# Performance work log

Hardware: AMD Instinct MI355X
Metric: run time of the kernel (lower is better)

## Reference

```python
import jax, jax.numpy as jnp
import numpy as np

NEG_SLOPE_MLP = 0.1   # F.leaky_relu(x, 0.1) used throughout the repo
NEG_SLOPE_GAT = 0.2   # PyG GATv2Conv default negative_slope
HEADS = 2
OUT = 8


def lrelu(x):
    return jax.nn.leaky_relu(x, NEG_SLOPE_MLP)


def gatv2_conv(x, src, dst, e_attr, wl, bl, wr, br, we, att, bias):
    """PyG-style GATv2Conv with edge features, concat heads.
    x: [N, Din], src/dst: [E], e_attr: [E, 2]
    wl/wr: [heads*out, Din], we: [heads*out, 2], att: [heads, out], bias: [heads*out]
    """
    N = x.shape[0]
    xl = (x @ wl.T + bl).reshape(N, HEADS, OUT)   # source transform
    xr = (x @ wr.T + br).reshape(N, HEADS, OUT)   # target transform
    e = (e_attr @ we.T).reshape(-1, HEADS, OUT)
    m = jax.nn.leaky_relu(xl[src] + xr[dst] + e, NEG_SLOPE_GAT)   # [E, H, O]
    logits = jnp.einsum('ehd,hd->eh', m, att)                      # [E, H]
    # numerically-stable segment softmax over incoming edges of each dst node
    mx = jax.ops.segment_max(logits, dst, num_segments=N)          # [N, H]
    a = jnp.exp(logits - mx[dst])
    denom = jax.ops.segment_sum(a, dst, num_segments=N)
    alpha = a / (denom[dst] + 1e-16)                               # [E, H]
    out = jax.ops.segment_sum(xl[src] * alpha[..., None], dst, num_segments=N)
    return out.reshape(N, HEADS * OUT) + bias                      # [N, 16]


def setup_inputs() -> dict:
    key = jax.random.key(0)
    ks = iter(jax.random.split(key, 64))
    N, E = 250000, 5000000
    inp = {
        'x': jax.random.normal(next(ks), (N, 3), jnp.float32),
        'edge_index': jax.random.randint(next(ks), (2, E), 0, N, jnp.int32),
        'edge_attr': jax.random.normal(next(ks), (E, 2), jnp.float32),
        'meta_data': jax.random.normal(next(ks), (6,), jnp.float32),
    }
    shapes = dict(
        ft1_w=(8, 3), ft1_b=(8,), ft2_w=(8, 8), ft2_b=(8,),
        g1_wl=(16, 8), g1_bl=(16,), g1_wr=(16, 8), g1_br=(16,), g1_we=(16, 2), g1_att=(2, 8), g1_bias=(16,),
        g2_wl=(16, 16), g2_bl=(16,), g2_wr=(16, 16), g2_br=(16,), g2_we=(16, 2), g2_att=(2, 8), g2_bias=(16,),
        sp1_w=(64, 16), sp1_b=(64,), sp2_w=(16, 64), sp2_b=(16,),
        me_w=(8, 6), me_b=(8,),
        fc1_w=(24, 24), fc1_b=(24,), fc2_w=(8, 24), fc2_b=(8,), fc3_w=(3, 8), fc3_b=(3,),
    )
    for name, shp in shapes.items():
        inp[name] = 0.2 * jax.random.normal(next(ks), shp, jnp.float32)
    return inp


def reference(x, edge_index, edge_attr, meta_data,
              ft1_w, ft1_b, ft2_w, ft2_b,
              g1_wl, g1_bl, g1_wr, g1_br, g1_we, g1_att, g1_bias,
              g2_wl, g2_bl, g2_wr, g2_br, g2_we, g2_att, g2_bias,
              sp1_w, sp1_b, sp2_w, sp2_b, me_w, me_b,
              fc1_w, fc1_b, fc2_w, fc2_b, fc3_w, fc3_b):
    src, dst = edge_index[0], edge_index[1]
    # tiny per-node MLP feature transform
    h = lrelu(x @ ft1_w.T + ft1_b)
    h = lrelu(h @ ft2_w.T + ft2_b)                              # [N, 8]
    # 2-layer GATv2 block (activation between layers)
    h = gatv2_conv(h, src, dst, edge_attr, g1_wl, g1_bl, g1_wr, g1_br, g1_we, g1_att, g1_bias)
    h = lrelu(h)
    h = gatv2_conv(h, src, dst, edge_attr, g2_wl, g2_bl, g2_wr, g2_br, g2_we, g2_att, g2_bias)  # [N, 16]
    # sum pool over all nodes + small MLP
    p = h.sum(axis=0)                                           # [16]
    p = lrelu(p @ sp1_w.T + sp1_b)
    p = p @ sp2_w.T + sp2_b                                     # [16]
    # meta data encoder
    m = lrelu(meta_data @ me_w.T + me_b)                        # [8]
    z = jnp.concatenate([p, m], axis=0)                         # [24]
    z = lrelu(z @ fc1_w.T + fc1_b)
    z = lrelu(z @ fc2_w.T + fc2_b)
    # dropout is identity in eval/reference mode
    z = z @ fc3_w.T + fc3_b                                     # [3]
    return jax.nn.softmax(z[None, :], axis=1)                   # [1, 3]
```

## Files before the change

### kernel.cpp

```cpp
#include <hip/hip_runtime.h>
#include <hip/hip_bf16.h>
#include <hip/hip_fp16.h>
#include <math.h>


#define HO 16
#define BSHIFT 8
#define BNODES 256
#define PT 512
#define PCHUNK 6144
#define CAP2 6016

typedef __attribute__((ext_vector_type(2))) float v2f;

__device__ __forceinline__ float lrelu(float x, float s) { return x > 0.f ? x : s * x; }

__device__ __forceinline__ uint2 pack_fp8x8(const float* v) {
    int a = __builtin_amdgcn_cvt_pk_fp8_f32(v[0], v[1], 0, false);
    a     = __builtin_amdgcn_cvt_pk_fp8_f32(v[2], v[3], a, true);
    int b = __builtin_amdgcn_cvt_pk_fp8_f32(v[4], v[5], 0, false);
    b     = __builtin_amdgcn_cvt_pk_fp8_f32(v[6], v[7], b, true);
    return make_uint2((unsigned int)a, (unsigned int)b);
}

__device__ __forceinline__ void unpack_fp8x8(uint2 u, float* v) {
    v2f f0 = __builtin_amdgcn_cvt_pk_f32_fp8((int)u.x, false);
    v2f f1 = __builtin_amdgcn_cvt_pk_f32_fp8((int)u.x, true);
    v2f f2 = __builtin_amdgcn_cvt_pk_f32_fp8((int)u.y, false);
    v2f f3 = __builtin_amdgcn_cvt_pk_f32_fp8((int)u.y, true);
    v[0]=f0.x; v[1]=f0.y; v[2]=f1.x; v[3]=f1.y;
    v[4]=f2.x; v[5]=f2.y; v[6]=f3.x; v[7]=f3.y;
}

__global__ void __launch_bounds__(256) node_l1(
    const float* __restrict__ x,
    const float* __restrict__ ft1_w, const float* __restrict__ ft1_b,
    const float* __restrict__ ft2_w, const float* __restrict__ ft2_b,
    const float* __restrict__ wl, const float* __restrict__ bl,
    const float* __restrict__ wr, const float* __restrict__ br,
    uint2* __restrict__ xlA, float* __restrict__ xr, int N)
{
    int n = blockIdx.x * 256 + threadIdx.x;
    if (n >= N) return;
    float x0 = x[3*n], x1 = x[3*n+1], x2 = x[3*n+2];
    float h1[8];
#pragma unroll
    for (int j = 0; j < 8; j++) {
        float a = ft1_w[3*j]*x0 + ft1_w[3*j+1]*x1 + ft1_w[3*j+2]*x2 + ft1_b[j];
        h1[j] = lrelu(a, 0.1f);
    }
    float h2[8];
#pragma unroll
    for (int j = 0; j < 8; j++) {
        float a = ft2_b[j];
#pragma unroll
        for (int k = 0; k < 8; k++) a += ft2_w[8*j+k]*h1[k];
        h2[j] = lrelu(a, 0.1f);
    }
    float ol[HO], orr[HO];
#pragma unroll
    for (int j = 0; j < HO; j++) {
        float a = bl[j], b = br[j];
#pragma unroll
        for (int k = 0; k < 8; k++) { a += wl[8*j+k]*h2[k]; b += wr[8*j+k]*h2[k]; }
        ol[j] = a; orr[j] = b;
    }
    uint2 p0 = pack_fp8x8(ol);
    uint2 p1 = pack_fp8x8(ol + 8);
    ((uint4*)xlA)[n] = make_uint4(p0.x, p0.y, p1.x, p1.y);
    float4* xr4 = (float4*)(xr + (size_t)n*HO);
#pragma unroll
    for (int q = 0; q < 4; q++)
        xr4[q] = make_float4(orr[4*q], orr[4*q+1], orr[4*q+2], orr[4*q+3]);
}

__global__ void __launch_bounds__(256) k_binit(int* __restrict__ bcur)
{
    int b = blockIdx.x * 256 + threadIdx.x;
    if (b < 1024) bcur[b] = b * CAP2;
}

__global__ void __launch_bounds__(PT) k_part(
    const int* __restrict__ src, const int* __restrict__ dst,
    const float* __restrict__ eattr, int* __restrict__ bcur,
    uint2* __restrict__ grecs, int E)
{
    __shared__ int hist[1024], lofs[1024], gofs[1024], lcur[1024];
    __shared__ int scan_s[PT];
    __shared__ uint2 srecs[PCHUNK];
    __shared__ unsigned short bid[PCHUNK];
    int t = threadIdx.x;
    int base = blockIdx.x * PCHUNK;
    int cnt = E - base; if (cnt > PCHUNK) cnt = PCHUNK;

    for (int b = t; b < 1024; b += PT) hist[b] = 0;
    __syncthreads();
    for (int i = t; i < cnt; i += PT)
        atomicAdd(&hist[dst[base + i] >> BSHIFT], 1);
    __syncthreads();
    int h0 = hist[2*t], h1 = hist[2*t+1];
    int pair = h0 + h1;
    scan_s[t] = pair;
    __syncthreads();
    for (int off = 1; off < PT; off <<= 1) {
        int add = (t >= off) ? scan_s[t - off] : 0;
        __syncthreads();
        scan_s[t] += add;
        __syncthreads();
    }
    int pbase = scan_s[t] - pair;
    lofs[2*t]   = pbase;
    lofs[2*t+1] = pbase + h0;
    __syncthreads();
    for (int b = t; b < 1024; b += PT) {
        int c = hist[b];
        int g = (c > 0) ? atomicAdd(&bcur[b], c) : 0;
        gofs[b] = g - lofs[b];
        lcur[b] = 0;
    }
    __syncthreads();
    for (int i = t; i < cnt; i += PT) {
        int e = base + i;
        int d = dst[e];
        int b = d >> BSHIFT;
        float2 ea = ((const float2*)eattr)[e];
        __half2 hv = __floats2half2_rn(ea.x, ea.y);
        unsigned int eb = *reinterpret_cast<unsigned int*>(&hv);
        int q = atomicAdd(&lcur[b], 1);
        int idx = lofs[b] + q;
        srecs[idx] = make_uint2(((unsigned int)src[e] << 8) | (unsigned int)(d & (BNODES-1)), eb);
        bid[idx] = (unsigned short)b;
    }
    __syncthreads();
    for (int i = t; i < cnt; i += PT) {
        int b = bid[i];
        int pos = gofs[b] + i;
        if (pos < (b + 1) * CAP2) grecs[pos] = srecs[i];
    }
}

__global__ void __launch_bounds__(256) k_fine(
    const int* __restrict__ bcur, uint2* recs,
    int* __restrict__ rowS, int* __restrict__ rowE, int N)
{
    __shared__ uint2 rout[CAP2];
    __shared__ int lhist[256], lsc[256], lcur2[256];
    int b = blockIdx.x;
    int bstart = b * CAP2;
    int cnt = bcur[b] - bstart;
    if (cnt > CAP2) cnt = CAP2;
    if (cnt < 0) cnt = 0;
    int t = threadIdx.x;
    lhist[t] = 0;
    __syncthreads();
    for (int i = t; i < cnt; i += 256)
        atomicAdd(&lhist[recs[bstart + i].x & (BNODES-1)], 1);
    __syncthreads();
    int v = lhist[t];
    lsc[t] = v;
    __syncthreads();
    for (int off = 1; off < 256; off <<= 1) {
        int add = (t >= off) ? lsc[t - off] : 0;
        __syncthreads();
        lsc[t] += add;
        __syncthreads();
    }
    int ex = lsc[t] - v;
    lcur2[t] = ex;
    int n = (b << BSHIFT) + t;
    if (n < N) { rowS[n] = bstart + ex; rowE[n] = bstart + ex + v; }
    __syncthreads();
    for (int i = t; i < cnt; i += 256) {
        uint2 r = recs[bstart + i];
        int p = atomicAdd(&lcur2[r.x & (BNODES-1)], 1);
        rout[p] = make_uint2(r.x >> 8, r.y);
    }
    __syncthreads();
    for (int i = t; i < cnt; i += 256)
        recs[bstart + i] = rout[i];
}

struct AggState { float m, s, acc[8]; };

__device__ __forceinline__ void agg_edge(
    AggState& st, const float* va, const float* xd,
    const float* w0, const float* w1, const float* at,
    float ea0, float ea1)
{
    float lg = 0.f;
#pragma unroll
    for (int o = 0; o < 8; o++) {
        float mv = va[o] + xd[o] + (w0[o]*ea0 + w1[o]*ea1);
        mv = mv > 0.f ? mv : 0.2f*mv;
        lg += mv * at[o];
    }
    float nm = fmaxf(st.m, lg);
    float sc = __expf(st.m - nm);
    float wv = __expf(lg - nm);
    st.s = st.s*sc + wv;
#pragma unroll
    for (int o = 0; o < 8; o++) st.acc[o] = st.acc[o]*sc + wv*va[o];
    st.m = nm;
}

__device__ __forceinline__ void agg_node_head(
    int n, int h,
    const int* __restrict__ rowS, const int* __restrict__ rowE,
    const uint2* __restrict__ recs,
    const uint2* __restrict__ xl8, const float* __restrict__ xr,
    const float* __restrict__ we, const float* __restrict__ att,
    const float* __restrict__ bias, float* out)
{
    int kb = h*8;
    float xd[8], w0[8], w1[8], at[8];
    {
        const float4* xrp = (const float4*)(xr + (size_t)n*HO + kb);
        float4 d0 = xrp[0], d1 = xrp[1];
        xd[0]=d0.x; xd[1]=d0.y; xd[2]=d0.z; xd[3]=d0.w;
        xd[4]=d1.x; xd[5]=d1.y; xd[6]=d1.z; xd[7]=d1.w;
    }
#pragma unroll
    for (int o = 0; o < 8; o++) {
        w0[o] = we[2*(kb+o)];
        w1[o] = we[2*(kb+o)+1];
        at[o] = att[kb+o];
    }
    AggState st;
    st.m = -INFINITY; st.s = 0.f;
#pragma unroll
    for (int o = 0; o < 8; o++) st.acc[o] = 0.f;

    int i = rowS[n], end = rowE[n];
    for (; i + 4 <= end; i += 4) {
        uint2 rA = recs[i], rB = recs[i+1], rC = recs[i+2], rD = recs[i+3];
        uint2 gA = xl8[(size_t)rA.x*2 + h];
        uint2 gB = xl8[(size_t)rB.x*2 + h];
        uint2 gC = xl8[(size_t)rC.x*2 + h];
        uint2 gD = xl8[(size_t)rD.x*2 + h];
        float vA[8], vB[8], vC[8], vD[8];
        unpack_fp8x8(gA, vA); unpack_fp8x8(gB, vB);
        unpack_fp8x8(gC, vC); unpack_fp8x8(gD, vD);
        __half2 hA = *reinterpret_cast<__half2*>(&rA.y);
        __half2 hB = *reinterpret_cast<__half2*>(&rB.y);
        __half2 hC = *reinterpret_cast<__half2*>(&rC.y);
        __half2 hD = *reinterpret_cast<__half2*>(&rD.y);
        agg_edge(st, vA, xd, w0, w1, at, __low2float(hA), __high2float(hA));
        agg_edge(st, vB, xd, w0, w1, at, __low2float(hB), __high2float(hB));
        agg_edge(st, vC, xd, w0, w1, at, __low2float(hC), __high2float(hC));
        agg_edge(st, vD, xd, w0, w1, at, __low2float(hD), __high2float(hD));
    }
    for (; i < end; i++) {
        uint2 rA = recs[i];
        uint2 gA = xl8[(size_t)rA.x*2 + h];
        float vA[8];
        unpack_fp8x8(gA, vA);
        __half2 hA = *reinterpret_cast<__half2*>(&rA.y);
        agg_edge(st, vA, xd, w0, w1, at, __low2float(hA), __high2float(hA));
    }
    float inv = 1.f/(st.s + 1e-16f);
#pragma unroll
    for (int o = 0; o < 8; o++) out[o] = st.acc[o]*inv + bias[kb+o];
}

__global__ void __launch_bounds__(256) node_agg_l1(
    const int* __restrict__ rowS, const int* __restrict__ rowE,
    const uint2* __restrict__ recs,
    const uint2* __restrict__ xlA, float* xr,
    const float* __restrict__ we, const float* __restrict__ att,
    const float* __restrict__ bias,
    const float* __restrict__ wl2, const float* __restrict__ bl2,
    const float* __restrict__ wr2, const float* __restrict__ br2,
    uint2* __restrict__ xlB, int N)
{
    int tid = blockIdx.x * 256 + threadIdx.x;
    int n = tid >> 1, h = tid & 1;
    if (n >= N) return;
    int kb = h*8;
    float out[8];
    agg_node_head(n, h, rowS, rowE, recs, xlA, xr, we, att, bias, out);
    float hh[8];
#pragma unroll
    for (int o = 0; o < 8; o++) hh[o] = lrelu(out[o], 0.1f);
    float hfull[HO];
#pragma unroll
    for (int o = 0; o < 8; o++) {
        float hp = __shfl_xor(hh[o], 1, 64);
        hfull[kb + o] = hh[o];
        hfull[(kb ^ 8) + o] = hp;
    }
    float ol[8], orr[8];
#pragma unroll
    for (int jo = 0; jo < 8; jo++) {
        int j = kb + jo;
        float a = bl2[j], b = br2[j];
#pragma unroll
        for (int k = 0; k < HO; k++) { a += wl2[HO*j+k]*hfull[k]; b += wr2[HO*j+k]*hfull[k]; }
        ol[jo] = a; orr[jo] = b;
    }
    xlB[(size_t)n*2 + h] = pack_fp8x8(ol);
    float4* xr4 = (float4*)(xr + (size_t)n*HO + kb);
    xr4[0] = make_float4(orr[0], orr[1], orr[2], orr[3]);
    xr4[1] = make_float4(orr[4], orr[5], orr[6], orr[7]);
}

__global__ void __launch_bounds__(256) node_agg_l2(
    const int* __restrict__ rowS, const int* __restrict__ rowE,
    const uint2* __restrict__ recs,
    const uint2* __restrict__ xlB, const float* __restrict__ xr,
    const float* __restrict__ we, const float* __restrict__ att,
    const float* __restrict__ bias, float* __restrict__ partials, int pstride, int N)
{
    int tid = blockIdx.x * 256 + threadIdx.x;
    int n = tid >> 1, h = tid & 1;
    float out[8];
    if (n < N) {
        agg_node_head(n, h, rowS, rowE, recs, xlB, xr, we, att, bias, out);
    } else {
#pragma unroll
        for (int o = 0; o < 8; o++) out[o] = 0.f;
    }
#pragma unroll
    for (int off = 32; off >= 2; off >>= 1) {
#pragma unroll
        for (int o = 0; o < 8; o++) out[o] += __shfl_down(out[o], off, 64);
    }
    __shared__ float sm[4][2][8];
    int wave = threadIdx.x >> 6, lane = threadIdx.x & 63;
    if (lane < 2) {
#pragma unroll
        for (int o = 0; o < 8; o++) sm[wave][lane][o] = out[o];
    }
    __syncthreads();
    if (threadIdx.x < 16) {
        int hh = threadIdx.x >> 3, oo = threadIdx.x & 7;
        float t = sm[0][hh][oo] + sm[1][hh][oo] + sm[2][hh][oo] + sm[3][hh][oo];
        partials[(size_t)(hh*8 + oo) * pstride + blockIdx.x] = t;
    }
}

__global__ void __launch_bounds__(256) k_reduce(
    const float* __restrict__ partials, int pstride, int nparts,
    float* __restrict__ pool)
{
    __shared__ float s[256];
    int c = blockIdx.x;
    int t = threadIdx.x;
    const float* col = partials + (size_t)c * pstride;
    float acc = 0.f;
    for (int r = t; r < nparts; r += 256) acc += col[r];
    s[t] = acc;
    __syncthreads();
#pragma unroll
    for (int off = 128; off > 0; off >>= 1) {
        if (t < off) s[t] += s[t + off];
        __syncthreads();
    }
    if (t == 0) pool[c] = s[0];
}

__global__ void __launch_bounds__(64) final_mlp(
    const float* __restrict__ pool, const float* __restrict__ meta,
    const float* __restrict__ sp1_w, const float* __restrict__ sp1_b,
    const float* __restrict__ sp2_w, const float* __restrict__ sp2_b,
    const float* __restrict__ me_w, const float* __restrict__ me_b,
    const float* __restrict__ fc1_w, const float* __restrict__ fc1_b,
    const float* __restrict__ fc2_w, const float* __restrict__ fc2_b,
    const float* __restrict__ fc3_w, const float* __restrict__ fc3_b,
    float* __restrict__ out)
{
    __shared__ float s1[64], zb[24], z1[24], z2[8];
    int t = threadIdx.x;
    {
        float acc = sp1_b[t];
        for (int k = 0; k < 16; k++) acc += pool[k]*sp1_w[t*16+k];
        s1[t] = lrelu(acc, 0.1f);
    }
    __syncthreads();
    if (t < 16) {
        float acc = sp2_b[t];
        for (int k = 0; k < 64; k++) acc += s1[k]*sp2_w[t*64+k];
        zb[t] = acc;
    } else if (t < 24) {
        int j = t - 16;
        float acc = me_b[j];
        for (int k = 0; k < 6; k++) acc += meta[k]*me_w[j*6+k];
        zb[t] = lrelu(acc, 0.1f);
    }
    __syncthreads();
    if (t < 24) {
        float acc = fc1_b[t];
        for (int k = 0; k < 24; k++) acc += zb[k]*fc1_w[t*24+k];
        z1[t] = lrelu(acc, 0.1f);
    }
    __syncthreads();
    if (t < 8) {
        float acc = fc2_b[t];
        for (int k = 0; k < 24; k++) acc += z1[k]*fc2_w[t*24+k];
        z2[t] = lrelu(acc, 0.1f);
    }
    __syncthreads();
    if (t == 0) {
        float z3[3]; float mxv = -1e30f;
        for (int j = 0; j < 3; j++) {
            float acc = fc3_b[j];
            for (int k = 0; k < 8; k++) acc += z2[k]*fc3_w[j*8+k];
            z3[j] = acc; mxv = fmaxf(mxv, acc);
        }
        float s = 0.f;
        for (int j = 0; j < 3; j++) { z3[j] = __expf(z3[j]-mxv); s += z3[j]; }
        for (int j = 0; j < 3; j++) out[j] = z3[j]/s;
    }
}

extern "C" void kernel_launch(void* const* d_in, const int* in_sizes, int n_in,
                              void* d_out, int out_size, void* d_ws, size_t ws_size,
                              hipStream_t stream)
{
    const float* x      = (const float*)d_in[0];
    const int*   eidx   = (const int*)  d_in[1];
    const float* eattr  = (const float*)d_in[2];
    const float* meta   = (const float*)d_in[3];
    const float* ft1_w  = (const float*)d_in[4];
    const float* ft1_b  = (const float*)d_in[5];
    const float* ft2_w  = (const float*)d_in[6];
    const float* ft2_b  = (const float*)d_in[7];
    const float* g1_wl  = (const float*)d_in[8];
    const float* g1_bl  = (const float*)d_in[9];
    const float* g1_wr  = (const float*)d_in[10];
    const float* g1_br  = (const float*)d_in[11];
    const float* g1_we  = (const float*)d_in[12];
    const float* g1_att = (const float*)d_in[13];
    const float* g1_bias= (const float*)d_in[14];
    const float* g2_wl  = (const float*)d_in[15];
    const float* g2_bl  = (const float*)d_in[16];
    const float* g2_wr  = (const float*)d_in[17];
    const float* g2_br  = (const float*)d_in[18];
    const float* g2_we  = (const float*)d_in[19];
    const float* g2_att = (const float*)d_in[20];
    const float* g2_bias= (const float*)d_in[21];
    const float* sp1_w  = (const float*)d_in[22];
    const float* sp1_b  = (const float*)d_in[23];
    const float* sp2_w  = (const float*)d_in[24];
    const float* sp2_b  = (const float*)d_in[25];
    const float* me_w   = (const float*)d_in[26];
    const float* me_b   = (const float*)d_in[27];
    const float* fc1_w  = (const float*)d_in[28];
    const float* fc1_b  = (const float*)d_in[29];
    const float* fc2_w  = (const float*)d_in[30];
    const float* fc2_b  = (const float*)d_in[31];
    const float* fc3_w  = (const float*)d_in[32];
    const float* fc3_b  = (const float*)d_in[33];
    float* out = (float*)d_out;

    const int N = in_sizes[0] / 3;
    const int E = in_sizes[2] / 2;
    const int* src = eidx;
    const int* dst = eidx + E;

    const int BN    = (N + 255) / 256;
    const int BN2   = (2*N + 255) / 256;
    const int NBUCK = (N + BNODES - 1) >> BSHIFT;
    const int BP    = (E + PCHUNK - 1) / PCHUNK;
    const int pstride = (BN2 + 63) & ~63;

    char* w = (char*)d_ws;
    size_t off = 0;
    auto take = [&](size_t bytes) { size_t o = off; off += (bytes + 255) & ~(size_t)255; return o; };
    int*    rowS     = (int*)   (w + take((size_t)4*N));
    int*    rowE     = (int*)   (w + take((size_t)4*N));
    int*    bcur     = (int*)   (w + take(4096));
    float*  pool     = (float*) (w + take(64));
    float*  partials = (float*) (w + take((size_t)4*16*pstride));
    uint2*  recs     = (uint2*) (w + take((size_t)8*NBUCK*CAP2));
    uint2*  xlA      = (uint2*) (w + take((size_t)16*N));
    uint2*  xlB      = (uint2*) (w + take((size_t)16*N));
    float*  xr       = (float*) (w + take((size_t)64*N));

    node_l1<<<BN, 256, 0, stream>>>(x, ft1_w, ft1_b, ft2_w, ft2_b,
                                    g1_wl, g1_bl, g1_wr, g1_br, xlA, xr, N);
    k_binit<<<4, 256, 0, stream>>>(bcur);
    k_part<<<BP, PT, 0, stream>>>(src, dst, eattr, bcur, recs, E);
    k_fine<<<NBUCK, 256, 0, stream>>>(bcur, recs, rowS, rowE, N);

    node_agg_l1<<<BN2, 256, 0, stream>>>(rowS, rowE, recs, xlA, xr,
                                         g1_we, g1_att, g1_bias,
                                         g2_wl, g2_bl, g2_wr, g2_br, xlB, N);
    node_agg_l2<<<BN2, 256, 0, stream>>>(rowS, rowE, recs, xlB, xr,
                                         g2_we, g2_att, g2_bias, partials, pstride, N);
    k_reduce<<<16, 256, 0, stream>>>(partials, pstride, BN2, pool);
    final_mlp<<<1, 64, 0, stream>>>(pool, meta, sp1_w, sp1_b, sp2_w, sp2_b,
                                    me_w, me_b, fc1_w, fc1_b, fc2_w, fc2_b,
                                    fc3_w, fc3_b, out);
}
```

Measured before the change: 424.7 us.

## Split each node-head edge loop across four lanes with online-softmax merge

The aggregation kernels now give each (node, head) pair four lanes instead of one. Each lane processes a strided subset of the incoming edges and keeps a partial online-softmax state, and the partial states are combined with xor-shuffle merges. The second-layer projection is split so that each sub-lane computes two output channels, and the fp8 pieces are assembled through shuffles. Non-temporal loads and stores are added for the edge records and xr. The aim is more parallelism and memory-level concurrency on the degree-20 gather loops, at the cost of extra shuffle/exp merge work and a larger grid and partials array.

```diff
diff --git a/kernel.cpp b/kernel.cpp
--- a/kernel.cpp
+++ b/kernel.cpp
@@ -12,6 +12,8 @@
 #define CAP2 6016
 
 typedef __attribute__((ext_vector_type(2))) float v2f;
+typedef __attribute__((ext_vector_type(4))) float v4f;
+typedef __attribute__((ext_vector_type(2))) unsigned int v2u;
 
 __device__ __forceinline__ float lrelu(float x, float s) { return x > 0.f ? x : s * x; }
 
@@ -32,6 +34,11 @@
     v[4]=f2.x; v[5]=f2.y; v[6]=f3.x; v[7]=f3.y;
 }
 
+__device__ __forceinline__ uint2 ntload_u2(const uint2* p) {
+    v2u v = __builtin_nontemporal_load((const v2u*)p);
+    return make_uint2(v.x, v.y);
+}
+
 __global__ void __launch_bounds__(256) node_l1(
     const float* __restrict__ x,
     const float* __restrict__ ft1_w, const float* __restrict__ ft1_b,
@@ -68,10 +75,12 @@
     uint2 p0 = pack_fp8x8(ol);
     uint2 p1 = pack_fp8x8(ol + 8);
     ((uint4*)xlA)[n] = make_uint4(p0.x, p0.y, p1.x, p1.y);
-    float4* xr4 = (float4*)(xr + (size_t)n*HO);
-#pragma unroll
-    for (int q = 0; q < 4; q++)
-        xr4[q] = make_float4(orr[4*q], orr[4*q+1], orr[4*q+2], orr[4*q+3]);
+    v4f* xr4 = (v4f*)(xr + (size_t)n*HO);
+#pragma unroll
+    for (int q = 0; q < 4; q++) {
+        v4f v; v.x = orr[4*q]; v.y = orr[4*q+1]; v.z = orr[4*q+2]; v.w = orr[4*q+3];
+        __builtin_nontemporal_store(v, xr4 + q);
+    }
 }
 
 __global__ void __launch_bounds__(256) k_binit(int* __restrict__ bcur)
@@ -203,19 +212,36 @@
     st.m = nm;
 }
 
-__device__ __forceinline__ void agg_node_head(
-    int n, int h,
+__device__ __forceinline__ void merge_xor(AggState& st, int mask)
+{
+    float pm = __shfl_xor(st.m, mask, 64);
+    float ps = __shfl_xor(st.s, mask, 64);
+    float pacc[8];
+#pragma unroll
+    for (int o = 0; o < 8; o++) pacc[o] = __shfl_xor(st.acc[o], mask, 64);
+    float nm = fmaxf(st.m, pm);
+    float e1 = __expf(st.m - nm);
+    float e2 = __expf(pm - nm);
+    st.s = st.s*e1 + ps*e2;
+#pragma unroll
+    for (int o = 0; o < 8; o++) st.acc[o] = st.acc[o]*e1 + pacc[o]*e2;
+    st.m = nm;
+}
+
+__device__ __forceinline__ void agg_partial(
+    int n, int h, int sub,
     const int* __restrict__ rowS, const int* __restrict__ rowE,
     const uint2* __restrict__ recs,
     const uint2* __restrict__ xl8, const float* __restrict__ xr,
     const float* __restrict__ we, const float* __restrict__ att,
-    const float* __restrict__ bias, float* out)
+    AggState& st)
 {
     int kb = h*8;
     float xd[8], w0[8], w1[8], at[8];
     {
-        const float4* xrp = (const float4*)(xr + (size_t)n*HO + kb);
-        float4 d0 = xrp[0], d1 = xrp[1];
+        const v4f* xrp = (const v4f*)(xr + (size_t)n*HO + kb);
+        v4f d0 = __builtin_nontemporal_load(xrp);
+        v4f d1 = __builtin_nontemporal_load(xrp + 1);
         xd[0]=d0.x; xd[1]=d0.y; xd[2]=d0.z; xd[3]=d0.w;
         xd[4]=d1.x; xd[5]=d1.y; xd[6]=d1.z; xd[7]=d1.w;
     }
@@ -225,41 +251,31 @@
         w1[o] = we[2*(kb+o)+1];
         at[o] = att[kb+o];
     }
-    AggState st;
-    st.m = -INFINITY; st.s = 0.f;
+    st.m = -1e30f; st.s = 0.f;
 #pragma unroll
     for (int o = 0; o < 8; o++) st.acc[o] = 0.f;
 
-    int i = rowS[n], end = rowE[n];
-    for (; i + 4 <= end; i += 4) {
-        uint2 rA = recs[i], rB = recs[i+1], rC = recs[i+2], rD = recs[i+3];
+    int i = rowS[n] + sub, end = rowE[n];
+    for (; i + 4 < end; i += 8) {
+        uint2 rA = ntload_u2(&recs[i]);
+        uint2 rB = ntload_u2(&recs[i+4]);
         uint2 gA = xl8[(size_t)rA.x*2 + h];
         uint2 gB = xl8[(size_t)rB.x*2 + h];
-        uint2 gC = xl8[(size_t)rC.x*2 + h];
-        uint2 gD = xl8[(size_t)rD.x*2 + h];
-        float vA[8], vB[8], vC[8], vD[8];
+        float vA[8], vB[8];
         unpack_fp8x8(gA, vA); unpack_fp8x8(gB, vB);
-        unpack_fp8x8(gC, vC); unpack_fp8x8(gD, vD);
         __half2 hA = *reinterpret_cast<__half2*>(&rA.y);
         __half2 hB = *reinterpret_cast<__half2*>(&rB.y);
-        __half2 hC = *reinterpret_cast<__half2*>(&rC.y);
-        __half2 hD = *reinterpret_cast<__half2*>(&rD.y);
         agg_edge(st, vA, xd, w0, w1, at, __low2float(hA), __high2float(hA));
         agg_edge(st, vB, xd, w0, w1, at, __low2float(hB), __high2float(hB));
-        agg_edge(st, vC, xd, w0, w1, at, __low2float(hC), __high2float(hC));
-        agg_edge(st, vD, xd, w0, w1, at, __low2float(hD), __high2float(hD));
-    }
-    for (; i < end; i++) {
-        uint2 rA = recs[i];
+    }
+    if (i < end) {
+        uint2 rA = ntload_u2(&recs[i]);
         uint2 gA = xl8[(size_t)rA.x*2 + h];
         float vA[8];
         unpack_fp8x8(gA, vA);
         __half2 hA = *reinterpret_cast<__half2*>(&rA.y);
         agg_edge(st, vA, xd, w0, w1, at, __low2float(hA), __high2float(hA));
     }
-    float inv = 1.f/(st.s + 1e-16f);
-#pragma unroll
-    for (int o = 0; o < 8; o++) out[o] = st.acc[o]*inv + bias[kb+o];
 }
 
 __global__ void __launch_bounds__(256) node_agg_l1(
@@ -273,34 +289,47 @@
     uint2* __restrict__ xlB, int N)
 {
     int tid = blockIdx.x * 256 + threadIdx.x;
-    int n = tid >> 1, h = tid & 1;
+    int n = tid >> 3, h = (tid >> 2) & 1, sub = tid & 3;
     if (n >= N) return;
     int kb = h*8;
-    float out[8];
-    agg_node_head(n, h, rowS, rowE, recs, xlA, xr, we, att, bias, out);
+    AggState st;
+    agg_partial(n, h, sub, rowS, rowE, recs, xlA, xr, we, att, st);
+    merge_xor(st, 1);
+    merge_xor(st, 2);
+    float inv = 1.f/(st.s + 1e-16f);
     float hh[8];
 #pragma unroll
-    for (int o = 0; o < 8; o++) hh[o] = lrelu(out[o], 0.1f);
+    for (int o = 0; o < 8; o++) hh[o] = lrelu(st.acc[o]*inv + bias[kb+o], 0.1f);
     float hfull[HO];
 #pragma unroll
     for (int o = 0; o < 8; o++) {
-        float hp = __shfl_xor(hh[o], 1, 64);
+        float hp = __shfl_xor(hh[o], 4, 64);
         hfull[kb + o] = hh[o];
         hfull[(kb ^ 8) + o] = hp;
     }
-    float ol[8], orr[8];
-#pragma unroll
-    for (int jo = 0; jo < 8; jo++) {
-        int j = kb + jo;
-        float a = bl2[j], b = br2[j];
-#pragma unroll
-        for (int k = 0; k < HO; k++) { a += wl2[HO*j+k]*hfull[k]; b += wr2[HO*j+k]*hfull[k]; }
-        ol[jo] = a; orr[jo] = b;
-    }
-    xlB[(size_t)n*2 + h] = pack_fp8x8(ol);
-    float4* xr4 = (float4*)(xr + (size_t)n*HO + kb);
-    xr4[0] = make_float4(orr[0], orr[1], orr[2], orr[3]);
-    xr4[1] = make_float4(orr[4], orr[5], orr[6], orr[7]);
+    int j0 = kb + 2*sub;
+    float a0 = bl2[j0], a1 = bl2[j0+1], b0 = br2[j0], b1 = br2[j0+1];
+#pragma unroll
+    for (int k = 0; k < HO; k++) {
+        float hk = hfull[k];
+        a0 += wl2[HO*j0 + k]     * hk;
+        a1 += wl2[HO*(j0+1) + k] * hk;
+        b0 += wr2[HO*j0 + k]     * hk;
+        b1 += wr2[HO*(j0+1) + k] * hk;
+    }
+    {
+        v2f v; v.x = b0; v.y = b1;
+        __builtin_nontemporal_store(v, (v2f*)(xr + (size_t)n*HO + kb + 2*sub));
+    }
+    int piece = __builtin_amdgcn_cvt_pk_fp8_f32(a0, a1, 0, false);
+    unsigned int pw = ((unsigned int)piece & 0xFFFFu) << ((sub & 1) * 16);
+    unsigned int px = (sub < 2) ? pw : 0u;
+    unsigned int py = (sub < 2) ? 0u : pw;
+    px |= (unsigned int)__shfl_xor((int)px, 1, 64);
+    py |= (unsigned int)__shfl_xor((int)py, 1, 64);
+    px |= (unsigned int)__shfl_xor((int)px, 2, 64);
+    py |= (unsigned int)__shfl_xor((int)py, 2, 64);
+    if (sub == 0) xlB[(size_t)n*2 + h] = make_uint2(px, py);
 }
 
 __global__ void __launch_bounds__(256) node_agg_l2(
@@ -311,24 +340,32 @@
     const float* __restrict__ bias, float* __restrict__ partials, int pstride, int N)
 {
     int tid = blockIdx.x * 256 + threadIdx.x;
-    int n = tid >> 1, h = tid & 1;
+    int n = tid >> 3, h = (tid >> 2) & 1, sub = tid & 3;
     float out[8];
+#pragma unroll
+    for (int o = 0; o < 8; o++) out[o] = 0.f;
     if (n < N) {
-        agg_node_head(n, h, rowS, rowE, recs, xlB, xr, we, att, bias, out);
-    } else {
-#pragma unroll
-        for (int o = 0; o < 8; o++) out[o] = 0.f;
-    }
-#pragma unroll
-    for (int off = 32; off >= 2; off >>= 1) {
+        AggState st;
+        agg_partial(n, h, sub, rowS, rowE, recs, xlB, xr, we, att, st);
+        merge_xor(st, 1);
+        merge_xor(st, 2);
+        if (sub == 0) {
+            float inv = 1.f/(st.s + 1e-16f);
+            int kb = h*8;
+#pragma unroll
+            for (int o = 0; o < 8; o++) out[o] = st.acc[o]*inv + bias[kb+o];
+        }
+    }
+#pragma unroll
+    for (int off = 32; off >= 8; off >>= 1) {
 #pragma unroll
         for (int o = 0; o < 8; o++) out[o] += __shfl_down(out[o], off, 64);
     }
     __shared__ float sm[4][2][8];
     int wave = threadIdx.x >> 6, lane = threadIdx.x & 63;
-    if (lane < 2) {
-#pragma unroll
-        for (int o = 0; o < 8; o++) sm[wave][lane][o] = out[o];
+    if (lane == 0 || lane == 4) {
+#pragma unroll
+        for (int o = 0; o < 8; o++) sm[wave][lane >> 2][o] = out[o];
     }
     __syncthreads();
     if (threadIdx.x < 16) {
@@ -458,10 +495,10 @@
     const int* dst = eidx + E;
 
     const int BN    = (N + 255) / 256;
-    const int BN2   = (2*N + 255) / 256;
+    const int BN8   = (8*N + 255) / 256;
     const int NBUCK = (N + BNODES - 1) >> BSHIFT;
     const int BP    = (E + PCHUNK - 1) / PCHUNK;
-    const int pstride = (BN2 + 63) & ~63;
+    const int pstride = (BN8 + 63) & ~63;
 
     char* w = (char*)d_ws;
     size_t off = 0;
@@ -482,12 +519,12 @@
     k_part<<<BP, PT, 0, stream>>>(src, dst, eattr, bcur, recs, E);
     k_fine<<<NBUCK, 256, 0, stream>>>(bcur, recs, rowS, rowE, N);
 
-    node_agg_l1<<<BN2, 256, 0, stream>>>(rowS, rowE, recs, xlA, xr,
+    node_agg_l1<<<BN8, 256, 0, stream>>>(rowS, rowE, recs, xlA, xr,
                                          g1_we, g1_att, g1_bias,
                                          g2_wl, g2_bl, g2_wr, g2_br, xlB, N);
-    node_agg_l2<<<BN2, 256, 0, stream>>>(rowS, rowE, recs, xlB, xr,
+    node_agg_l2<<<BN8, 256, 0, stream>>>(rowS, rowE, recs, xlB, xr,
                                          g2_we, g2_att, g2_bias, partials, pstride, N);
-    k_reduce<<<16, 256, 0, stream>>>(partials, pstride, BN2, pool);
+    k_reduce<<<16, 256, 0, stream>>>(partials, pstride, BN8, pool);
     final_mlp<<<1, 64, 0, stream>>>(pool, meta, sp1_w, sp1_b, sp2_w, sp2_b,
                                     me_w, me_b, fc1_w, fc1_b, fc2_w, fc2_b,
                                     fc3_w, fc3_b, out);
```

Measured after the change: 466.1 us. +9.7%, slower.

## Process both attention heads per thread and use nontemporal loads/stores

Applied to the files above, without the earlier changes.

The aggregation kernels now assign one thread per node instead of one per (node, head). Each edge record is read once and one 16-byte fp8 gather fetches both heads. This removes the duplicated record reads and the cross-lane shuffle between head threads, but halves the thread count and raises register pressure, which can reduce occupancy and latency hiding for the irregular gathers. Nontemporal hints are also added on the streamed edge records and the xr row loads/stores.

```diff
diff --git a/kernel.cpp b/kernel.cpp
--- a/kernel.cpp
+++ b/kernel.cpp
@@ -12,6 +12,8 @@
 #define CAP2 6016
 
 typedef __attribute__((ext_vector_type(2))) float v2f;
+typedef __attribute__((ext_vector_type(4))) float v4f;
+typedef __attribute__((ext_vector_type(2))) unsigned int v2u;
 
 __device__ __forceinline__ float lrelu(float x, float s) { return x > 0.f ? x : s * x; }
 
@@ -23,13 +25,24 @@
     return make_uint2((unsigned int)a, (unsigned int)b);
 }
 
-__device__ __forceinline__ void unpack_fp8x8(uint2 u, float* v) {
+__device__ __forceinline__ void unpack_fp8x16(uint4 u, float* v) {
     v2f f0 = __builtin_amdgcn_cvt_pk_f32_fp8((int)u.x, false);
     v2f f1 = __builtin_amdgcn_cvt_pk_f32_fp8((int)u.x, true);
     v2f f2 = __builtin_amdgcn_cvt_pk_f32_fp8((int)u.y, false);
     v2f f3 = __builtin_amdgcn_cvt_pk_f32_fp8((int)u.y, true);
-    v[0]=f0.x; v[1]=f0.y; v[2]=f1.x; v[3]=f1.y;
-    v[4]=f2.x; v[5]=f2.y; v[6]=f3.x; v[7]=f3.y;
+    v2f f4 = __builtin_amdgcn_cvt_pk_f32_fp8((int)u.z, false);
+    v2f f5 = __builtin_amdgcn_cvt_pk_f32_fp8((int)u.z, true);
+    v2f f6 = __builtin_amdgcn_cvt_pk_f32_fp8((int)u.w, false);
+    v2f f7 = __builtin_amdgcn_cvt_pk_f32_fp8((int)u.w, true);
+    v[0]=f0.x;  v[1]=f0.y;  v[2]=f1.x;  v[3]=f1.y;
+    v[4]=f2.x;  v[5]=f2.y;  v[6]=f3.x;  v[7]=f3.y;
+    v[8]=f4.x;  v[9]=f4.y;  v[10]=f5.x; v[11]=f5.y;
+    v[12]=f6.x; v[13]=f6.y; v[14]=f7.x; v[15]=f7.y;
+}
+
+__device__ __forceinline__ uint2 ntload_u2(const uint2* p) {
+    v2u v = __builtin_nontemporal_load((const v2u*)p);
+    return make_uint2(v.x, v.y);
 }
 
 __global__ void __launch_bounds__(256) node_l1(
@@ -68,10 +81,12 @@
     uint2 p0 = pack_fp8x8(ol);
     uint2 p1 = pack_fp8x8(ol + 8);
     ((uint4*)xlA)[n] = make_uint4(p0.x, p0.y, p1.x, p1.y);
-    float4* xr4 = (float4*)(xr + (size_t)n*HO);
-#pragma unroll
-    for (int q = 0; q < 4; q++)
-        xr4[q] = make_float4(orr[4*q], orr[4*q+1], orr[4*q+2], orr[4*q+3]);
+    v4f* xr4 = (v4f*)(xr + (size_t)n*HO);
+#pragma unroll
+    for (int q = 0; q < 4; q++) {
+        v4f v; v.x = orr[4*q]; v.y = orr[4*q+1]; v.z = orr[4*q+2]; v.w = orr[4*q+3];
+        __builtin_nontemporal_store(v, xr4 + q);
+    }
 }
 
 __global__ void __launch_bounds__(256) k_binit(int* __restrict__ bcur)
@@ -203,138 +218,163 @@
     st.m = nm;
 }
 
-__device__ __forceinline__ void agg_node_head(
-    int n, int h,
+__device__ __forceinline__ void agg_node_both(
+    int n,
     const int* __restrict__ rowS, const int* __restrict__ rowE,
     const uint2* __restrict__ recs,
-    const uint2* __restrict__ xl8, const float* __restrict__ xr,
+    const uint4* __restrict__ xl16, const float* __restrict__ xr,
     const float* __restrict__ we, const float* __restrict__ att,
-    const float* __restrict__ bias, float* out)
-{
-    int kb = h*8;
-    float xd[8], w0[8], w1[8], at[8];
+    AggState& s0, AggState& s1)
+{
+    float xd[16], w0[16], w1[16], at[16];
     {
-        const float4* xrp = (const float4*)(xr + (size_t)n*HO + kb);
-        float4 d0 = xrp[0], d1 = xrp[1];
-        xd[0]=d0.x; xd[1]=d0.y; xd[2]=d0.z; xd[3]=d0.w;
-        xd[4]=d1.x; xd[5]=d1.y; xd[6]=d1.z; xd[7]=d1.w;
-    }
-#pragma unroll
-    for (int o = 0; o < 8; o++) {
-        w0[o] = we[2*(kb+o)];
-        w1[o] = we[2*(kb+o)+1];
-        at[o] = att[kb+o];
-    }
-    AggState st;
-    st.m = -INFINITY; st.s = 0.f;
-#pragma unroll
-    for (int o = 0; o < 8; o++) st.acc[o] = 0.f;
+        const v4f* xrp = (const v4f*)(xr + (size_t)n*HO);
+#pragma unroll
+        for (int q = 0; q < 4; q++) {
+            v4f d = __builtin_nontemporal_load(xrp + q);
+            xd[4*q]=d.x; xd[4*q+1]=d.y; xd[4*q+2]=d.z; xd[4*q+3]=d.w;
+        }
+    }
+#pragma unroll
+    for (int o = 0; o < 16; o++) {
+        w0[o] = we[2*o];
+        w1[o] = we[2*o+1];
+        at[o] = att[o];
+    }
+    s0.m = -1e30f; s0.s = 0.f;
+    s1.m = -1e30f; s1.s = 0.f;
+#pragma unroll
+    for (int o = 0; o < 8; o++) { s0.acc[o] = 0.f; s1.acc[o] = 0.f; }
 
     int i = rowS[n], end = rowE[n];
     for (; i + 4 <= end; i += 4) {
-        uint2 rA = recs[i], rB = recs[i+1], rC = recs[i+2], rD = recs[i+3];
-        uint2 gA = xl8[(size_t)rA.x*2 + h];
-        uint2 gB = xl8[(size_t)rB.x*2 + h];
-        uint2 gC = xl8[(size_t)rC.x*2 + h];
-        uint2 gD = xl8[(size_t)rD.x*2 + h];
-        float vA[8], vB[8], vC[8], vD[8];
-        unpack_fp8x8(gA, vA); unpack_fp8x8(gB, vB);
-        unpack_fp8x8(gC, vC); unpack_fp8x8(gD, vD);
+        uint2 rA = ntload_u2(&recs[i]);
+        uint2 rB = ntload_u2(&recs[i+1]);
+        uint2 rC = ntload_u2(&recs[i+2]);
+        uint2 rD = ntload_u2(&recs[i+3]);
+        uint4 gA = xl16[rA.x];
+        uint4 gB = xl16[rB.x];
+        uint4 gC = xl16[rC.x];
+        uint4 gD = xl16[rD.x];
+        {
+            float v[16]; unpack_fp8x16(gA, v);
+            __half2 hA = *reinterpret_cast<__half2*>(&rA.y);
+            float e0 = __low2float(hA), e1 = __high2float(hA);
+            agg_edge(s0, v,     xd,     w0,     w1,     at,     e0, e1);
+            agg_edge(s1, v + 8, xd + 8, w0 + 8, w1 + 8, at + 8, e0, e1);
+        }
+        {
+            float v[16]; unpack_fp8x16(gB, v);
+            __half2 hB = *reinterpret_cast<__half2*>(&rB.y);
+            float e0 = __low2float(hB), e1 = __high2float(hB);
+            agg_edge(s0, v,     xd,     w0,     w1,     at,     e0, e1);
+            agg_edge(s1, v + 8, xd + 8, w0 + 8, w1 + 8, at + 8, e0, e1);
+        }
+        {
+            float v[16]; unpack_fp8x16(gC, v);
+            __half2 hC = *reinterpret_cast<__half2*>(&rC.y);
+            float e0 = __low2float(hC), e1 = __high2float(hC);
+            agg_edge(s0, v,     xd,     w0,     w1,     at,     e0, e1);
+            agg_edge(s1, v + 8, xd + 8, w0 + 8, w1 + 8, at + 8, e0, e1);
+        }
+        {
+            float v[16]; unpack_fp8x16(gD, v);
+            __half2 hD = *reinterpret_cast<__half2*>(&rD.y);
+            float e0 = __low2float(hD), e1 = __high2float(hD);
+            agg_edge(s0, v,     xd,     w0,     w1,     at,     e0, e1);
+            agg_edge(s1, v + 8, xd + 8, w0 + 8, w1 + 8, at + 8, e0, e1);
+        }
+    }
+    for (; i < end; i++) {
+        uint2 rA = ntload_u2(&recs[i]);
+        uint4 gA = xl16[rA.x];
+        float v[16]; unpack_fp8x16(gA, v);
         __half2 hA = *reinterpret_cast<__half2*>(&rA.y);
-        __half2 hB = *reinterpret_cast<__half2*>(&rB.y);
-        __half2 hC = *reinterpret_cast<__half2*>(&rC.y);
-        __half2 hD = *reinterpret_cast<__half2*>(&rD.y);
-        agg_edge(st, vA, xd, w0, w1, at, __low2float(hA), __high2float(hA));
-        agg_edge(st, vB, xd, w0, w1, at, __low2float(hB), __high2float(hB));
-        agg_edge(st, vC, xd, w0, w1, at, __low2float(hC), __high2float(hC));
-        agg_edge(st, vD, xd, w0, w1, at, __low2float(hD), __high2float(hD));
-    }
-    for (; i < end; i++) {
-        uint2 rA = recs[i];
-        uint2 gA = xl8[(size_t)rA.x*2 + h];
-        float vA[8];
-        unpack_fp8x8(gA, vA);
-        __half2 hA = *reinterpret_cast<__half2*>(&rA.y);
-        agg_edge(st, vA, xd, w0, w1, at, __low2float(hA), __high2float(hA));
-    }
-    float inv = 1.f/(st.s + 1e-16f);
-#pragma unroll
-    for (int o = 0; o < 8; o++) out[o] = st.acc[o]*inv + bias[kb+o];
+        float e0 = __low2float(hA), e1 = __high2float(hA);
+        agg_edge(s0, v,     xd,     w0,     w1,     at,     e0, e1);
+        agg_edge(s1, v + 8, xd + 8, w0 + 8, w1 + 8, at + 8, e0, e1);
+    }
 }
 
 __global__ void __launch_bounds__(256) node_agg_l1(
     const int* __restrict__ rowS, const int* __restrict__ rowE,
     const uint2* __restrict__ recs,
-    const uint2* __restrict__ xlA, float* xr,
+    const uint4* __restrict__ xlA, float* xr,
     const float* __restrict__ we, const float* __restrict__ att,
     const float* __restrict__ bias,
     const float* __restrict__ wl2, const float* __restrict__ bl2,
     const float* __restrict__ wr2, const float* __restrict__ br2,
-    uint2* __restrict__ xlB, int N)
-{
-    int tid = blockIdx.x * 256 + threadIdx.x;
-    int n = tid >> 1, h = tid & 1;
+    uint4* __restrict__ xlB, int N)
+{
+    int n = blockIdx.x * 256 + threadIdx.x;
     if (n >= N) return;
-    int kb = h*8;
-    float out[8];
-    agg_node_head(n, h, rowS, rowE, recs, xlA, xr, we, att, bias, out);
-    float hh[8];
-#pragma unroll
-    for (int o = 0; o < 8; o++) hh[o] = lrelu(out[o], 0.1f);
+    AggState s0, s1;
+    agg_node_both(n, rowS, rowE, recs, xlA, xr, we, att, s0, s1);
+    float inv0 = 1.f/(s0.s + 1e-16f);
+    float inv1 = 1.f/(s1.s + 1e-16f);
     float hfull[HO];
 #pragma unroll
     for (int o = 0; o < 8; o++) {
-        float hp = __shfl_xor(hh[o], 1, 64);
-        hfull[kb + o] = hh[o];
-        hfull[(kb ^ 8) + o] = hp;
-    }
-    float ol[8], orr[8];
-#pragma unroll
-    for (int jo = 0; jo < 8; jo++) {
-        int j = kb + jo;
+        hfull[o]     = lrelu(s0.acc[o]*inv0 + bias[o],     0.1f);
+        hfull[8 + o] = lrelu(s1.acc[o]*inv1 + bias[8 + o], 0.1f);
+    }
+    float ol[HO], orr[HO];
+#pragma unroll
+    for (int j = 0; j < HO; j++) {
         float a = bl2[j], b = br2[j];
 #pragma unroll
         for (int k = 0; k < HO; k++) { a += wl2[HO*j+k]*hfull[k]; b += wr2[HO*j+k]*hfull[k]; }
-        ol[jo] = a; orr[jo] = b;
-    }
-    xlB[(size_t)n*2 + h] = pack_fp8x8(ol);
-    float4* xr4 = (float4*)(xr + (size_t)n*HO + kb);
-    xr4[0] = make_float4(orr[0], orr[1], orr[2], orr[3]);
-    xr4[1] = make_float4(orr[4], orr[5], orr[6], orr[7]);
+        ol[j] = a; orr[j] = b;
+    }
+    uint2 q0 = pack_fp8x8(ol);
+    uint2 q1 = pack_fp8x8(ol + 8);
+    xlB[n] = make_uint4(q0.x, q0.y, q1.x, q1.y);
+    v4f* xr4 = (v4f*)(xr + (size_t)n*HO);
+#pragma unroll
+    for (int q = 0; q < 4; q++) {
+        v4f v; v.x = orr[4*q]; v.y = orr[4*q+1]; v.z = orr[4*q+2]; v.w = orr[4*q+3];
+        __builtin_nontemporal_store(v, xr4 + q);
+    }
 }
 
 __global__ void __launch_bounds__(256) node_agg_l2(
     const int* __restrict__ rowS, const int* __restrict__ rowE,
     const uint2* __restrict__ recs,
-    const uint2* __restrict__ xlB, const float* __restrict__ xr,
+    const uint4* __restrict__ xlB, const float* __restrict__ xr,
     const float* __restrict__ we, const float* __restrict__ att,
     const float* __restrict__ bias, float* __restrict__ partials, int pstride, int N)
 {
-    int tid = blockIdx.x * 256 + threadIdx.x;
-    int n = tid >> 1, h = tid & 1;
-    float out[8];
+    int n = blockIdx.x * 256 + threadIdx.x;
+    float out[HO];
+#pragma unroll
+    for (int o = 0; o < HO; o++) out[o] = 0.f;
     if (n < N) {
-        agg_node_head(n, h, rowS, rowE, recs, xlB, xr, we, att, bias, out);
-    } else {
-#pragma unroll
-        for (int o = 0; o < 8; o++) out[o] = 0.f;
-    }
-#pragma unroll
-    for (int off = 32; off >= 2; off >>= 1) {
-#pragma unroll
-        for (int o = 0; o < 8; o++) out[o] += __shfl_down(out[o], off, 64);
-    }
-    __shared__ float sm[4][2][8];
+        AggState s0, s1;
+        agg_node_both(n, rowS, rowE, recs, xlB, xr, we, att, s0, s1);
+        float inv0 = 1.f/(s0.s + 1e-16f);
+        float inv1 = 1.f/(s1.s + 1e-16f);
+#pragma unroll
+        for (int o = 0; o < 8; o++) {
+            out[o]     = s0.acc[o]*inv0 + bias[o];
+            out[8 + o] = s1.acc[o]*inv1 + bias[8 + o];
+        }
+    }
+#pragma unroll
+    for (int off = 32; off >= 1; off >>= 1) {
+#pragma unroll
+        for (int o = 0; o < HO; o++) out[o] += __shfl_down(out[o], off, 64);
+    }
+    __shared__ float sm[4][HO];
     int wave = threadIdx.x >> 6, lane = threadIdx.x & 63;
-    if (lane < 2) {
-#pragma unroll
-        for (int o = 0; o < 8; o++) sm[wave][lane][o] = out[o];
-    }
-    __syncthreads();
-    if (threadIdx.x < 16) {
-        int hh = threadIdx.x >> 3, oo = threadIdx.x & 7;
-        float t = sm[0][hh][oo] + sm[1][hh][oo] + sm[2][hh][oo] + sm[3][hh][oo];
-        partials[(size_t)(hh*8 + oo) * pstride + blockIdx.x] = t;
+    if (lane == 0) {
+#pragma unroll
+        for (int o = 0; o < HO; o++) sm[wave][o] = out[o];
+    }
+    __syncthreads();
+    if (threadIdx.x < HO) {
+        int oo = threadIdx.x;
+        float t = sm[0][oo] + sm[1][oo] + sm[2][oo] + sm[3][oo];
+        partials[(size_t)oo * pstride + blockIdx.x] = t;
     }
 }
 
@@ -458,10 +498,9 @@
     const int* dst = eidx + E;
 
     const int BN    = (N + 255) / 256;
-    const int BN2   = (2*N + 255) / 256;
     const int NBUCK = (N + BNODES - 1) >> BSHIFT;
     const int BP    = (E + PCHUNK - 1) / PCHUNK;
-    const int pstride = (BN2 + 63) & ~63;
+    const int pstride = (BN + 63) & ~63;
 
     char* w = (char*)d_ws;
     size_t off = 0;
@@ -472,22 +511,22 @@
     float*  pool     = (float*) (w + take(64));
     float*  partials = (float*) (w + take((size_t)4*16*pstride));
     uint2*  recs     = (uint2*) (w + take((size_t)8*NBUCK*CAP2));
-    uint2*  xlA      = (uint2*) (w + take((size_t)16*N));
-    uint2*  xlB      = (uint2*) (w + take((size_t)16*N));
+    uint4*  xlA      = (uint4*) (w + take((size_t)16*N));
+    uint4*  xlB      = (uint4*) (w + take((size_t)16*N));
     float*  xr       = (float*) (w + take((size_t)64*N));
 
     node_l1<<<BN, 256, 0, stream>>>(x, ft1_w, ft1_b, ft2_w, ft2_b,
-                                    g1_wl, g1_bl, g1_wr, g1_br, xlA, xr, N);
+                                    g1_wl, g1_bl, g1_wr, g1_br, (uint2*)xlA, xr, N);
     k_binit<<<4, 256, 0, stream>>>(bcur);
     k_part<<<BP, PT, 0, stream>>>(src, dst, eattr, bcur, recs, E);
     k_fine<<<NBUCK, 256, 0, stream>>>(bcur, recs, rowS, rowE, N);
 
-    node_agg_l1<<<BN2, 256, 0, stream>>>(rowS, rowE, recs, xlA, xr,
-                                         g1_we, g1_att, g1_bias,
-                                         g2_wl, g2_bl, g2_wr, g2_br, xlB, N);
-    node_agg_l2<<<BN2, 256, 0, stream>>>(rowS, rowE, recs, xlB, xr,
-                                         g2_we, g2_att, g2_bias, partials, pstride, N);
-    k_reduce<<<16, 256, 0, stream>>>(partials, pstride, BN2, pool);
+    node_agg_l1<<<BN, 256, 0, stream>>>(rowS, rowE, recs, xlA, xr,
+                                        g1_we, g1_att, g1_bias,
+                                        g2_wl, g2_bl, g2_wr, g2_br, xlB, N);
+    node_agg_l2<<<BN, 256, 0, stream>>>(rowS, rowE, recs, xlB, xr,
+                                        g2_we, g2_att, g2_bias, partials, pstride, N);
+    k_reduce<<<16, 256, 0, stream>>>(partials, pstride, BN, pool);
     final_mlp<<<1, 64, 0, stream>>>(pool, meta, sp1_w, sp1_b, sp2_w, sp2_b,
                                     me_w, me_b, fc1_w, fc1_b, fc2_w, fc2_b,
                                     fc3_w, fc3_b, out);
```

After: 441.0 us. +3.8%, slower.

## Stage block's edge gathers cooperatively into LDS before per-node softmax aggregation

Applied to the files above, without the earlier changes.

Each 128-node block now walks its contiguous CSR edge range in chunks. All 256 threads cooperatively load the edge records and gather the full 16-byte fp8 source feature rows into shared memory, so the gathers are coalesced and spread evenly. Each thread then reads its own node's edges for its head from LDS. This removes the per-thread serial dependent gather chains and the load imbalance from skewed degrees. The cost is extra syncthreads, LDS capacity limiting occupancy, and each gather now fetching both heads per edge.

```diff
diff --git a/kernel.cpp b/kernel.cpp
--- a/kernel.cpp
+++ b/kernel.cpp
@@ -10,8 +10,10 @@
 #define PT 512
 #define PCHUNK 6144
 #define CAP2 6016
+#define CAPB 1984
 
 typedef __attribute__((ext_vector_type(2))) float v2f;
+typedef __attribute__((ext_vector_type(4))) float v4f;
 
 __device__ __forceinline__ float lrelu(float x, float s) { return x > 0.f ? x : s * x; }
 
@@ -203,84 +205,90 @@
     st.m = nm;
 }
 
-__device__ __forceinline__ void agg_node_head(
-    int n, int h,
+__device__ __forceinline__ void agg_lds(
+    int t, int nblk0, int N,
     const int* __restrict__ rowS, const int* __restrict__ rowE,
-    const uint2* __restrict__ recs,
-    const uint2* __restrict__ xl8, const float* __restrict__ xr,
-    const float* __restrict__ we, const float* __restrict__ att,
-    const float* __restrict__ bias, float* out)
-{
-    int kb = h*8;
-    float xd[8], w0[8], w1[8], at[8];
-    {
-        const float4* xrp = (const float4*)(xr + (size_t)n*HO + kb);
-        float4 d0 = xrp[0], d1 = xrp[1];
-        xd[0]=d0.x; xd[1]=d0.y; xd[2]=d0.z; xd[3]=d0.w;
-        xd[4]=d1.x; xd[5]=d1.y; xd[6]=d1.z; xd[7]=d1.w;
-    }
-#pragma unroll
-    for (int o = 0; o < 8; o++) {
-        w0[o] = we[2*(kb+o)];
-        w1[o] = we[2*(kb+o)+1];
-        at[o] = att[kb+o];
-    }
-    AggState st;
-    st.m = -INFINITY; st.s = 0.f;
-#pragma unroll
-    for (int o = 0; o < 8; o++) st.acc[o] = 0.f;
-
-    int i = rowS[n], end = rowE[n];
-    for (; i + 4 <= end; i += 4) {
-        uint2 rA = recs[i], rB = recs[i+1], rC = recs[i+2], rD = recs[i+3];
-        uint2 gA = xl8[(size_t)rA.x*2 + h];
-        uint2 gB = xl8[(size_t)rB.x*2 + h];
-        uint2 gC = xl8[(size_t)rC.x*2 + h];
-        uint2 gD = xl8[(size_t)rD.x*2 + h];
-        float vA[8], vB[8], vC[8], vD[8];
-        unpack_fp8x8(gA, vA); unpack_fp8x8(gB, vB);
-        unpack_fp8x8(gC, vC); unpack_fp8x8(gD, vD);
-        __half2 hA = *reinterpret_cast<__half2*>(&rA.y);
-        __half2 hB = *reinterpret_cast<__half2*>(&rB.y);
-        __half2 hC = *reinterpret_cast<__half2*>(&rC.y);
-        __half2 hD = *reinterpret_cast<__half2*>(&rD.y);
-        agg_edge(st, vA, xd, w0, w1, at, __low2float(hA), __high2float(hA));
-        agg_edge(st, vB, xd, w0, w1, at, __low2float(hB), __high2float(hB));
-        agg_edge(st, vC, xd, w0, w1, at, __low2float(hC), __high2float(hC));
-        agg_edge(st, vD, xd, w0, w1, at, __low2float(hD), __high2float(hD));
-    }
-    for (; i < end; i++) {
-        uint2 rA = recs[i];
-        uint2 gA = xl8[(size_t)rA.x*2 + h];
-        float vA[8];
-        unpack_fp8x8(gA, vA);
-        __half2 hA = *reinterpret_cast<__half2*>(&rA.y);
-        agg_edge(st, vA, xd, w0, w1, at, __low2float(hA), __high2float(hA));
-    }
-    float inv = 1.f/(st.s + 1e-16f);
-#pragma unroll
-    for (int o = 0; o < 8; o++) out[o] = st.acc[o]*inv + bias[kb+o];
+    const uint2* __restrict__ recs, const uint4* __restrict__ xl16,
+    uint4* va_s, unsigned int* ea_s,
+    bool alive, int rs, int re, int h,
+    const float* xd, const float* w0, const float* w1, const float* at,
+    AggState& st)
+{
+    int nlast = nblk0 + 127; if (nlast > N - 1) nlast = N - 1;
+    int ebeg = rowS[nblk0];
+    int eend = rowE[nlast];
+    for (int cbase = ebeg; cbase < eend; cbase += CAPB) {
+        int ccnt = eend - cbase; if (ccnt > CAPB) ccnt = CAPB;
+        __syncthreads();
+        for (int j = t; j < ccnt; j += 256) {
+            uint2 r = recs[cbase + j];
+            va_s[j] = xl16[r.x];
+            ea_s[j] = r.y;
+        }
+        __syncthreads();
+        if (alive) {
+            int ls = rs > cbase ? rs : cbase;
+            int ce = cbase + ccnt;
+            int le = re < ce ? re : ce;
+            for (int i = ls; i < le; i++) {
+                int j = i - cbase;
+                const uint2* vp = reinterpret_cast<const uint2*>(va_s + j);
+                uint2 g = vp[h];
+                float v[8]; unpack_fp8x8(g, v);
+                unsigned int eb = ea_s[j];
+                __half2 h2 = *reinterpret_cast<__half2*>(&eb);
+                agg_edge(st, v, xd, w0, w1, at, __low2float(h2), __high2float(h2));
+            }
+        }
+    }
 }
 
 __global__ void __launch_bounds__(256) node_agg_l1(
     const int* __restrict__ rowS, const int* __restrict__ rowE,
     const uint2* __restrict__ recs,
-    const uint2* __restrict__ xlA, float* xr,
+    const uint4* __restrict__ xlA, float* xr,
     const float* __restrict__ we, const float* __restrict__ att,
     const float* __restrict__ bias,
     const float* __restrict__ wl2, const float* __restrict__ bl2,
     const float* __restrict__ wr2, const float* __restrict__ br2,
     uint2* __restrict__ xlB, int N)
 {
-    int tid = blockIdx.x * 256 + threadIdx.x;
+    __shared__ uint4 va_s[CAPB];
+    __shared__ unsigned int ea_s[CAPB];
+    int t = threadIdx.x;
+    int tid = blockIdx.x * 256 + t;
     int n = tid >> 1, h = tid & 1;
-    if (n >= N) return;
+    bool alive = (n < N);
     int kb = h*8;
-    float out[8];
-    agg_node_head(n, h, rowS, rowE, recs, xlA, xr, we, att, bias, out);
+    int rs = alive ? rowS[n] : 0;
+    int re = alive ? rowE[n] : 0;
+    float xd[8], w0[8], w1[8], at[8];
+    {
+        size_t nn = alive ? (size_t)n : 0;
+        const float4* xrp = (const float4*)(xr + nn*HO + kb);
+        float4 d0 = xrp[0], d1 = xrp[1];
+        xd[0]=d0.x; xd[1]=d0.y; xd[2]=d0.z; xd[3]=d0.w;
+        xd[4]=d1.x; xd[5]=d1.y; xd[6]=d1.z; xd[7]=d1.w;
+    }
+#pragma unroll
+    for (int o = 0; o < 8; o++) {
+        w0[o] = we[2*(kb+o)];
+        w1[o] = we[2*(kb+o)+1];
+        at[o] = att[kb+o];
+    }
+    AggState st;
+    st.m = -INFINITY; st.s = 0.f;
+#pragma unroll
+    for (int o = 0; o < 8; o++) st.acc[o] = 0.f;
+
+    agg_lds(t, blockIdx.x*128, N, rowS, rowE, recs, xlA, va_s, ea_s,
+            alive, rs, re, h, xd, w0, w1, at, st);
+    if (!alive) return;
+
+    float inv = 1.f/(st.s + 1e-16f);
     float hh[8];
 #pragma unroll
-    for (int o = 0; o < 8; o++) hh[o] = lrelu(out[o], 0.1f);
+    for (int o = 0; o < 8; o++) hh[o] = lrelu(st.acc[o]*inv + bias[kb+o], 0.1f);
     float hfull[HO];
 #pragma unroll
     for (int o = 0; o < 8; o++) {
@@ -306,15 +314,46 @@
 __global__ void __launch_bounds__(256) node_agg_l2(
     const int* __restrict__ rowS, const int* __restrict__ rowE,
     const uint2* __restrict__ recs,
-    const uint2* __restrict__ xlB, const float* __restrict__ xr,
+    const uint4* __restrict__ xlB, const float* __restrict__ xr,
     const float* __restrict__ we, const float* __restrict__ att,
     const float* __restrict__ bias, float* __restrict__ partials, int pstride, int N)
 {
-    int tid = blockIdx.x * 256 + threadIdx.x;
+    __shared__ uint4 va_s[CAPB];
+    __shared__ unsigned int ea_s[CAPB];
+    int t = threadIdx.x;
+    int tid = blockIdx.x * 256 + t;
     int n = tid >> 1, h = tid & 1;
+    bool alive = (n < N);
+    int kb = h*8;
+    int rs = alive ? rowS[n] : 0;
+    int re = alive ? rowE[n] : 0;
+    float xd[8], w0[8], w1[8], at[8];
+    {
+        size_t nn = alive ? (size_t)n : 0;
+        const float4* xrp = (const float4*)(xr + nn*HO + kb);
+        float4 d0 = xrp[0], d1 = xrp[1];
+        xd[0]=d0.x; xd[1]=d0.y; xd[2]=d0.z; xd[3]=d0.w;
+        xd[4]=d1.x; xd[5]=d1.y; xd[6]=d1.z; xd[7]=d1.w;
+    }
+#pragma unroll
+    for (int o = 0; o < 8; o++) {
+        w0[o] = we[2*(kb+o)];
+        w1[o] = we[2*(kb+o)+1];
+        at[o] = att[kb+o];
+    }
+    AggState st;
+    st.m = -INFINITY; st.s = 0.f;
+#pragma unroll
+    for (int o = 0; o < 8; o++) st.acc[o] = 0.f;
+
+    agg_lds(t, blockIdx.x*128, N, rowS, rowE, recs, xlB, va_s, ea_s,
+            alive, rs, re, h, xd, w0, w1, at, st);
+
     float out[8];
-    if (n < N) {
-        agg_node_head(n, h, rowS, rowE, recs, xlB, xr, we, att, bias, out);
+    if (alive) {
+        float inv = 1.f/(st.s + 1e-16f);
+#pragma unroll
+        for (int o = 0; o < 8; o++) out[o] = st.acc[o]*inv + bias[kb+o];
     } else {
 #pragma unroll
         for (int o = 0; o < 8; o++) out[o] = 0.f;
@@ -333,8 +372,8 @@
     __syncthreads();
     if (threadIdx.x < 16) {
         int hh = threadIdx.x >> 3, oo = threadIdx.x & 7;
-        float t = sm[0][hh][oo] + sm[1][hh][oo] + sm[2][hh][oo] + sm[3][hh][oo];
-        partials[(size_t)(hh*8 + oo) * pstride + blockIdx.x] = t;
+        float tt = sm[0][hh][oo] + sm[1][hh][oo] + sm[2][hh][oo] + sm[3][hh][oo];
+        partials[(size_t)(hh*8 + oo) * pstride + blockIdx.x] = tt;
     }
 }
 
@@ -482,10 +521,10 @@
     k_part<<<BP, PT, 0, stream>>>(src, dst, eattr, bcur, recs, E);
     k_fine<<<NBUCK, 256, 0, stream>>>(bcur, recs, rowS, rowE, N);
 
-    node_agg_l1<<<BN2, 256, 0, stream>>>(rowS, rowE, recs, xlA, xr,
+    node_agg_l1<<<BN2, 256, 0, stream>>>(rowS, rowE, recs, (const uint4*)xlA, xr,
                                          g1_we, g1_att, g1_bias,
                                          g2_wl, g2_bl, g2_wr, g2_br, xlB, N);
-    node_agg_l2<<<BN2, 256, 0, stream>>>(rowS, rowE, recs, xlB, xr,
+    node_agg_l2<<<BN2, 256, 0, stream>>>(rowS, rowE, recs, (const uint4*)xlB, xr,
                                          g2_we, g2_att, g2_bias, partials, pstride, N);
     k_reduce<<<16, 256, 0, stream>>>(partials, pstride, BN2, pool);
     final_mlp<<<1, 64, 0, stream>>>(pool, meta, sp1_w, sp1_b, sp2_w, sp2_b,
```

New measurement: 442.3 us. 1.04x slower.
